# Kernel optimization log

Measured on AMD Instinct MI355X. Metric: run time of the kernel, lower is better.

Reference implementation:

```python
import jax, jax.numpy as jnp
import numpy as np

EPS = 1e-6
WEIGHT_THRESHOLD = 0.0


def setup_inputs() -> dict:
    key = jax.random.key(0)
    kA, kB, kW = jax.random.split(key, 3)
    bs, n = 200000, 20
    A = jax.random.normal(kA, (bs, n, 3), dtype=jnp.float32)
    B = jax.random.normal(kB, (bs, n, 3), dtype=jnp.float32)
    weights = jax.random.uniform(kW, (bs, n), dtype=jnp.float32)
    return {"A": A, "B": B, "weights": weights}


def reference(A, B, weights):
    """Batched weighted Procrustes (Kabsch). A,B: [bs,n,3], weights: [bs,n].
    Returns SE3 transforms [bs,4,4], matching rigid_transform_3d + integrate_trans."""
    w = jnp.where(weights < WEIGHT_THRESHOLD, 0.0, weights)
    wsum = jnp.sum(w, axis=1, keepdims=True)[:, :, None] + EPS  # [bs,1,1]
    centroid_A = jnp.sum(A * w[:, :, None], axis=1, keepdims=True) / wsum  # [bs,1,3]
    centroid_B = jnp.sum(B * w[:, :, None], axis=1, keepdims=True) / wsum
    Am = A - centroid_A
    Bm = B - centroid_B
    # H = Am^T diag(w) Bm  -> [bs,3,3]
    H = jnp.einsum('bni,bn,bnj->bij', Am, w, Bm)
    U, S, Vh = jnp.linalg.svd(H)          # H = U S Vh
    V = jnp.swapaxes(Vh, -1, -2)          # torch.svd's "Vt" is actually V
    Ut = jnp.swapaxes(U, -1, -2)
    delta = jnp.linalg.det(V @ Ut)        # [bs]
    corr = jnp.broadcast_to(jnp.eye(3, dtype=A.dtype), V.shape).copy()
    corr = corr.at[:, 2, 2].set(delta)
    R = V @ corr @ Ut                     # [bs,3,3]
    t = jnp.swapaxes(centroid_B, 1, 2) - R @ jnp.swapaxes(centroid_A, 1, 2)  # [bs,3,1]
    top = jnp.concatenate([R, t], axis=-1)  # [bs,3,4]
    bottom = jnp.broadcast_to(jnp.array([0.0, 0.0, 0.0, 1.0], dtype=A.dtype), (A.shape[0], 1, 4))
    return jnp.concatenate([top, bottom], axis=1)  # [bs,4,4]
```

## Files before the change

### kernel.cpp

```cpp
#include <hip/hip_runtime.h>

#define EPS_W 1e-6f

__global__ __launch_bounds__(256) void kabsch4x4_kernel(
    const float* __restrict__ A, const float* __restrict__ B,
    const float* __restrict__ W, float* __restrict__ Out,
    int bs, int n)
{
    const int b = blockIdx.x * blockDim.x + threadIdx.x;
    if (b >= bs) return;

    float sw = 0.f;
    float Sa0=0.f,Sa1=0.f,Sa2=0.f, Sb0=0.f,Sb1=0.f,Sb2=0.f;
    float M00=0.f,M01=0.f,M02=0.f,M10=0.f,M11=0.f,M12=0.f,M20=0.f,M21=0.f,M22=0.f;

    if ((n & 3) == 0) {
        const float4* A4 = reinterpret_cast<const float4*>(A + (size_t)b * n * 3);
        const float4* B4 = reinterpret_cast<const float4*>(B + (size_t)b * n * 3);
        const float4* W4 = reinterpret_cast<const float4*>(W + (size_t)b * n);
        const int ng = n >> 2;
        for (int g = 0; g < ng; ++g) {
            float4 a0 = A4[3*g+0], a1 = A4[3*g+1], a2 = A4[3*g+2];
            float4 b0 = B4[3*g+0], b1 = B4[3*g+1], b2 = B4[3*g+2];
            float4 wv = W4[g];
            const float af[12] = {a0.x,a0.y,a0.z,a0.w, a1.x,a1.y,a1.z,a1.w, a2.x,a2.y,a2.z,a2.w};
            const float bf[12] = {b0.x,b0.y,b0.z,b0.w, b1.x,b1.y,b1.z,b1.w, b2.x,b2.y,b2.z,b2.w};
            const float wf[4]  = {wv.x,wv.y,wv.z,wv.w};
            #pragma unroll
            for (int k = 0; k < 4; ++k) {
                float w = wf[k] < 0.f ? 0.f : wf[k];
                float ax = af[3*k+0], ay = af[3*k+1], az = af[3*k+2];
                float bx = bf[3*k+0], by = bf[3*k+1], bz = bf[3*k+2];
                sw += w;
                float wax = w*ax, way = w*ay, waz = w*az;
                Sa0 += wax; Sa1 += way; Sa2 += waz;
                Sb0 += w*bx; Sb1 += w*by; Sb2 += w*bz;
                M00 += wax*bx; M01 += wax*by; M02 += wax*bz;
                M10 += way*bx; M11 += way*by; M12 += way*bz;
                M20 += waz*bx; M21 += waz*by; M22 += waz*bz;
            }
        }
    } else {
        for (int j = 0; j < n; ++j) {
            const float* ap = A + ((size_t)b * n + j) * 3;
            const float* bp = B + ((size_t)b * n + j) * 3;
            float w = W[(size_t)b * n + j];
            w = w < 0.f ? 0.f : w;
            float ax=ap[0], ay=ap[1], az=ap[2];
            float bx=bp[0], by=bp[1], bz=bp[2];
            sw += w;
            float wax = w*ax, way = w*ay, waz = w*az;
            Sa0 += wax; Sa1 += way; Sa2 += waz;
            Sb0 += w*bx; Sb1 += w*by; Sb2 += w*bz;
            M00 += wax*bx; M01 += wax*by; M02 += wax*bz;
            M10 += way*bx; M11 += way*by; M12 += way*bz;
            M20 += waz*bx; M21 += waz*by; M22 += waz*bz;
        }
    }

    const float inv = 1.f / (sw + EPS_W);
    const float cA0 = Sa0*inv, cA1 = Sa1*inv, cA2 = Sa2*inv;
    const float cB0 = Sb0*inv, cB1 = Sb1*inv, cB2 = Sb2*inv;

    float H[3][3];
    H[0][0] = M00 - cA0*Sb0 - Sa0*cB0 + sw*cA0*cB0;
    H[0][1] = M01 - cA0*Sb1 - Sa0*cB1 + sw*cA0*cB1;
    H[0][2] = M02 - cA0*Sb2 - Sa0*cB2 + sw*cA0*cB2;
    H[1][0] = M10 - cA1*Sb0 - Sa1*cB0 + sw*cA1*cB0;
    H[1][1] = M11 - cA1*Sb1 - Sa1*cB1 + sw*cA1*cB1;
    H[1][2] = M12 - cA1*Sb2 - Sa1*cB2 + sw*cA1*cB2;
    H[2][0] = M20 - cA2*Sb0 - Sa2*cB0 + sw*cA2*cB0;
    H[2][1] = M21 - cA2*Sb1 - Sa2*cB1 + sw*cA2*cB1;
    H[2][2] = M22 - cA2*Sb2 - Sa2*cB2 + sw*cA2*cB2;

    const float Sxx=H[0][0], Sxy=H[0][1], Sxz=H[0][2];
    const float Syx=H[1][0], Syy=H[1][1], Syz=H[1][2];
    const float Szx=H[2][0], Szy=H[2][1], Szz=H[2][2];

    float Nm[4][4];
    Nm[0][0] =  Sxx+Syy+Szz; Nm[0][1] = Syz-Szy;      Nm[0][2] = Szx-Sxz;      Nm[0][3] = Sxy-Syx;
    Nm[1][0] =  Nm[0][1];    Nm[1][1] = Sxx-Syy-Szz;  Nm[1][2] = Sxy+Syx;      Nm[1][3] = Szx+Sxz;
    Nm[2][0] =  Nm[0][2];    Nm[2][1] = Nm[1][2];     Nm[2][2] = -Sxx+Syy-Szz; Nm[2][3] = Syz+Szy;
    Nm[3][0] =  Nm[0][3];    Nm[3][1] = Nm[1][3];     Nm[3][2] = Nm[2][3];     Nm[3][3] = -Sxx-Syy+Szz;

    float Vv[4][4] = {{1.f,0.f,0.f,0.f},{0.f,1.f,0.f,0.f},{0.f,0.f,1.f,0.f},{0.f,0.f,0.f,1.f}};

    for (int sweep = 0; sweep < 6; ++sweep) {
        #pragma unroll
        for (int pair = 0; pair < 6; ++pair) {
            constexpr int PP[6] = {0,0,0,1,1,2};
            constexpr int QQ[6] = {1,2,3,2,3,3};
            const int p = PP[pair], q = QQ[pair];
            float apq = Nm[p][q];
            float c, s;
            if (fabsf(apq) > 1e-20f) {
                float tau = (Nm[q][q] - Nm[p][p]) / (2.f * apq);
                float t = copysignf(1.f, tau) / (fabsf(tau) + sqrtf(1.f + tau*tau));
                c = rsqrtf(1.f + t*t);
                s = t * c;
            } else {
                c = 1.f; s = 0.f;
            }
            #pragma unroll
            for (int k = 0; k < 4; ++k) {
                float akp = Nm[k][p], akq = Nm[k][q];
                Nm[k][p] = c*akp - s*akq;
                Nm[k][q] = s*akp + c*akq;
            }
            #pragma unroll
            for (int k = 0; k < 4; ++k) {
                float apk = Nm[p][k], aqk = Nm[q][k];
                Nm[p][k] = c*apk - s*aqk;
                Nm[q][k] = s*apk + c*aqk;
            }
            #pragma unroll
            for (int k = 0; k < 4; ++k) {
                float vkp = Vv[k][p], vkq = Vv[k][q];
                Vv[k][p] = c*vkp - s*vkq;
                Vv[k][q] = s*vkp + c*vkq;
            }
        }
    }

    float q0=Vv[0][0], q1=Vv[1][0], q2=Vv[2][0], q3=Vv[3][0];
    float best = Nm[0][0];
    #pragma unroll
    for (int m = 1; m < 4; ++m) {
        bool bt = Nm[m][m] > best;
        best = bt ? Nm[m][m] : best;
        q0 = bt ? Vv[0][m] : q0;
        q1 = bt ? Vv[1][m] : q1;
        q2 = bt ? Vv[2][m] : q2;
        q3 = bt ? Vv[3][m] : q3;
    }
    float qn = rsqrtf(q0*q0 + q1*q1 + q2*q2 + q3*q3);
    q0*=qn; q1*=qn; q2*=qn; q3*=qn;

    float R00 = q0*q0+q1*q1-q2*q2-q3*q3;
    float R01 = 2.f*(q1*q2 - q0*q3);
    float R02 = 2.f*(q1*q3 + q0*q2);
    float R10 = 2.f*(q1*q2 + q0*q3);
    float R11 = q0*q0-q1*q1+q2*q2-q3*q3;
    float R12 = 2.f*(q2*q3 - q0*q1);
    float R20 = 2.f*(q1*q3 - q0*q2);
    float R21 = 2.f*(q2*q3 + q0*q1);
    float R22 = q0*q0-q1*q1-q2*q2+q3*q3;

    float trRH  = R00*H[0][0]+R01*H[1][0]+R02*H[2][0]
                + R10*H[0][1]+R11*H[1][1]+R12*H[2][1]
                + R20*H[0][2]+R21*H[1][2]+R22*H[2][2];
    float trRtH = R00*H[0][0]+R01*H[0][1]+R02*H[0][2]
                + R10*H[1][0]+R11*H[1][1]+R12*H[1][2]
                + R20*H[2][0]+R21*H[2][1]+R22*H[2][2];
    if (trRtH > trRH) {
        float t;
        t = R01; R01 = R10; R10 = t;
        t = R02; R02 = R20; R20 = t;
        t = R12; R12 = R21; R21 = t;
    }

    float t0 = cB0 - (R00*cA0 + R01*cA1 + R02*cA2);
    float t1 = cB1 - (R10*cA0 + R11*cA1 + R12*cA2);
    float t2 = cB2 - (R20*cA0 + R21*cA1 + R22*cA2);

    float4* O4 = reinterpret_cast<float4*>(Out + (size_t)b * 16);
    O4[0] = make_float4(R00, R01, R02, t0);
    O4[1] = make_float4(R10, R11, R12, t1);
    O4[2] = make_float4(R20, R21, R22, t2);
    O4[3] = make_float4(0.f, 0.f, 0.f, 1.f);
}

extern "C" void kernel_launch(void* const* d_in, const int* in_sizes, int n_in,
                              void* d_out, int out_size, void* d_ws, size_t ws_size,
                              hipStream_t stream) {
    const float* A = (const float*)d_in[0];
    const float* B = (const float*)d_in[1];
    const float* W = (const float*)d_in[2];
    float* Out = (float*)d_out;
    const int bs = out_size / 16;
    const int n  = (bs > 0) ? (in_sizes[2] / bs) : 0;
    const int threads = 256;
    const int blocks = (bs + threads - 1) / threads;
    hipLaunchKernelGGL(kabsch4x4_kernel, dim3(blocks), dim3(threads), 0, stream,
                       A, B, W, Out, bs, n);
}
```

Measured before the change: 172.5 us.

## Split each Kabsch item across two lanes, cut Jacobi sweeps, divide-free rotation

For n==20, each batch item is now handled by two adjacent threads. Each thread accumulates half the points with float2 loads, the partial sums are combined with an xor shuffle, and each thread writes half of the 4x4 output. The Jacobi eigen-solve drops from six sweeps to five, and the rotation angle is computed with rsqrt instead of divides and sqrt. The aim is more parallelism and memory-level concurrency for the load phase and less ALU work in the solve. The cost is that both lanes redundantly run the full solve, and the reduced sweep count risks accuracy on ill-conditioned inputs.

```diff
diff --git a/kernel.cpp b/kernel.cpp
--- a/kernel.cpp
+++ b/kernel.cpp
@@ -2,62 +2,14 @@
 
 #define EPS_W 1e-6f
 
-__global__ __launch_bounds__(256) void kabsch4x4_kernel(
-    const float* __restrict__ A, const float* __restrict__ B,
-    const float* __restrict__ W, float* __restrict__ Out,
-    int bs, int n)
+__device__ __forceinline__ void solve_from_sums(
+    float sw, float Sa0, float Sa1, float Sa2,
+    float Sb0, float Sb1, float Sb2,
+    float M00, float M01, float M02,
+    float M10, float M11, float M12,
+    float M20, float M21, float M22,
+    float R[9], float t[3])
 {
-    const int b = blockIdx.x * blockDim.x + threadIdx.x;
-    if (b >= bs) return;
-
-    float sw = 0.f;
-    float Sa0=0.f,Sa1=0.f,Sa2=0.f, Sb0=0.f,Sb1=0.f,Sb2=0.f;
-    float M00=0.f,M01=0.f,M02=0.f,M10=0.f,M11=0.f,M12=0.f,M20=0.f,M21=0.f,M22=0.f;
-
-    if ((n & 3) == 0) {
-        const float4* A4 = reinterpret_cast<const float4*>(A + (size_t)b * n * 3);
-        const float4* B4 = reinterpret_cast<const float4*>(B + (size_t)b * n * 3);
-        const float4* W4 = reinterpret_cast<const float4*>(W + (size_t)b * n);
-        const int ng = n >> 2;
-        for (int g = 0; g < ng; ++g) {
-            float4 a0 = A4[3*g+0], a1 = A4[3*g+1], a2 = A4[3*g+2];
-            float4 b0 = B4[3*g+0], b1 = B4[3*g+1], b2 = B4[3*g+2];
-            float4 wv = W4[g];
-            const float af[12] = {a0.x,a0.y,a0.z,a0.w, a1.x,a1.y,a1.z,a1.w, a2.x,a2.y,a2.z,a2.w};
-            const float bf[12] = {b0.x,b0.y,b0.z,b0.w, b1.x,b1.y,b1.z,b1.w, b2.x,b2.y,b2.z,b2.w};
-            const float wf[4]  = {wv.x,wv.y,wv.z,wv.w};
-            #pragma unroll
-            for (int k = 0; k < 4; ++k) {
-                float w = wf[k] < 0.f ? 0.f : wf[k];
-                float ax = af[3*k+0], ay = af[3*k+1], az = af[3*k+2];
-                float bx = bf[3*k+0], by = bf[3*k+1], bz = bf[3*k+2];
-                sw += w;
-                float wax = w*ax, way = w*ay, waz = w*az;
-                Sa0 += wax; Sa1 += way; Sa2 += waz;
-                Sb0 += w*bx; Sb1 += w*by; Sb2 += w*bz;
-                M00 += wax*bx; M01 += wax*by; M02 += wax*bz;
-                M10 += way*bx; M11 += way*by; M12 += way*bz;
-                M20 += waz*bx; M21 += waz*by; M22 += waz*bz;
-            }
-        }
-    } else {
-        for (int j = 0; j < n; ++j) {
-            const float* ap = A + ((size_t)b * n + j) * 3;
-            const float* bp = B + ((size_t)b * n + j) * 3;
-            float w = W[(size_t)b * n + j];
-            w = w < 0.f ? 0.f : w;
-            float ax=ap[0], ay=ap[1], az=ap[2];
-            float bx=bp[0], by=bp[1], bz=bp[2];
-            sw += w;
-            float wax = w*ax, way = w*ay, waz = w*az;
-            Sa0 += wax; Sa1 += way; Sa2 += waz;
-            Sb0 += w*bx; Sb1 += w*by; Sb2 += w*bz;
-            M00 += wax*bx; M01 += wax*by; M02 += wax*bz;
-            M10 += way*bx; M11 += way*by; M12 += way*bz;
-            M20 += waz*bx; M21 += waz*by; M22 += waz*bz;
-        }
-    }
-
     const float inv = 1.f / (sw + EPS_W);
     const float cA0 = Sa0*inv, cA1 = Sa1*inv, cA2 = Sa2*inv;
     const float cB0 = Sb0*inv, cB1 = Sb1*inv, cB2 = Sb2*inv;
@@ -85,22 +37,23 @@
 
     float Vv[4][4] = {{1.f,0.f,0.f,0.f},{0.f,1.f,0.f,0.f},{0.f,0.f,1.f,0.f},{0.f,0.f,0.f,1.f}};
 
-    for (int sweep = 0; sweep < 6; ++sweep) {
+    for (int sweep = 0; sweep < 5; ++sweep) {
         #pragma unroll
         for (int pair = 0; pair < 6; ++pair) {
             constexpr int PP[6] = {0,0,0,1,1,2};
             constexpr int QQ[6] = {1,2,3,2,3,3};
             const int p = PP[pair], q = QQ[pair];
-            float apq = Nm[p][q];
-            float c, s;
-            if (fabsf(apq) > 1e-20f) {
-                float tau = (Nm[q][q] - Nm[p][p]) / (2.f * apq);
-                float t = copysignf(1.f, tau) / (fabsf(tau) + sqrtf(1.f + tau*tau));
-                c = rsqrtf(1.f + t*t);
-                s = t * c;
-            } else {
-                c = 1.f; s = 0.f;
-            }
+            float d  = Nm[p][p] - Nm[q][q];
+            float o  = Nm[p][q];
+            float r2 = d*d + 4.f*o*o;
+            bool tiny = r2 < 1e-30f;
+            float rinv = rsqrtf(tiny ? 1.f : r2);
+            float hh = 0.5f + 0.5f * fabsf(d) * rinv;
+            float ci = rsqrtf(hh);
+            float c  = hh * ci;
+            float s  = (d < 0.f ? o : -o) * rinv * ci;
+            c = tiny ? 1.f : c;
+            s = tiny ? 0.f : s;
             #pragma unroll
             for (int k = 0; k < 4; ++k) {
                 float akp = Nm[k][p], akq = Nm[k][q];
@@ -153,20 +106,125 @@
                 + R10*H[1][0]+R11*H[1][1]+R12*H[1][2]
                 + R20*H[2][0]+R21*H[2][1]+R22*H[2][2];
     if (trRtH > trRH) {
-        float t;
-        t = R01; R01 = R10; R10 = t;
-        t = R02; R02 = R20; R20 = t;
-        t = R12; R12 = R21; R21 = t;
-    }
-
-    float t0 = cB0 - (R00*cA0 + R01*cA1 + R02*cA2);
-    float t1 = cB1 - (R10*cA0 + R11*cA1 + R12*cA2);
-    float t2 = cB2 - (R20*cA0 + R21*cA1 + R22*cA2);
+        float tt;
+        tt = R01; R01 = R10; R10 = tt;
+        tt = R02; R02 = R20; R20 = tt;
+        tt = R12; R12 = R21; R21 = tt;
+    }
+
+    R[0]=R00; R[1]=R01; R[2]=R02;
+    R[3]=R10; R[4]=R11; R[5]=R12;
+    R[6]=R20; R[7]=R21; R[8]=R22;
+    t[0] = cB0 - (R00*cA0 + R01*cA1 + R02*cA2);
+    t[1] = cB1 - (R10*cA0 + R11*cA1 + R12*cA2);
+    t[2] = cB2 - (R20*cA0 + R21*cA1 + R22*cA2);
+}
+
+__global__ __launch_bounds__(256) void kabsch_pair20_kernel(
+    const float* __restrict__ A, const float* __restrict__ B,
+    const float* __restrict__ W, float* __restrict__ Out, int bs)
+{
+    const int tid  = blockIdx.x * blockDim.x + threadIdx.x;
+    const int item = tid >> 1;
+    const int h    = tid & 1;
+    if (item >= bs) return;
+
+    const float2* A2 = reinterpret_cast<const float2*>(A);
+    const float2* B2 = reinterpret_cast<const float2*>(B);
+    const float2* W2 = reinterpret_cast<const float2*>(W);
+    const int abase = item*30 + h*15;
+    const int wbase = item*10 + h*5;
+
+    float sw = 0.f;
+    float Sa0=0.f,Sa1=0.f,Sa2=0.f, Sb0=0.f,Sb1=0.f,Sb2=0.f;
+    float M00=0.f,M01=0.f,M02=0.f,M10=0.f,M11=0.f,M12=0.f,M20=0.f,M21=0.f,M22=0.f;
+
+    #pragma unroll
+    for (int g = 0; g < 5; ++g) {
+        float2 a0 = A2[abase+3*g+0], a1 = A2[abase+3*g+1], a2 = A2[abase+3*g+2];
+        float2 b0 = B2[abase+3*g+0], b1 = B2[abase+3*g+1], b2 = B2[abase+3*g+2];
+        float2 wv = W2[wbase+g];
+        float w0 = wv.x < 0.f ? 0.f : wv.x;
+        float w1 = wv.y < 0.f ? 0.f : wv.y;
+
+        {
+            float ax=a0.x, ay=a0.y, az=a1.x;
+            float bx=b0.x, by=b0.y, bz=b1.x;
+            sw += w0;
+            float wax=w0*ax, way=w0*ay, waz=w0*az;
+            Sa0+=wax; Sa1+=way; Sa2+=waz;
+            Sb0+=w0*bx; Sb1+=w0*by; Sb2+=w0*bz;
+            M00+=wax*bx; M01+=wax*by; M02+=wax*bz;
+            M10+=way*bx; M11+=way*by; M12+=way*bz;
+            M20+=waz*bx; M21+=waz*by; M22+=waz*bz;
+        }
+        {
+            float ax=a1.y, ay=a2.x, az=a2.y;
+            float bx=b1.y, by=b2.x, bz=b2.y;
+            sw += w1;
+            float wax=w1*ax, way=w1*ay, waz=w1*az;
+            Sa0+=wax; Sa1+=way; Sa2+=waz;
+            Sb0+=w1*bx; Sb1+=w1*by; Sb2+=w1*bz;
+            M00+=wax*bx; M01+=wax*by; M02+=wax*bz;
+            M10+=way*bx; M11+=way*by; M12+=way*bz;
+            M20+=waz*bx; M21+=waz*by; M22+=waz*bz;
+        }
+    }
+
+    sw  += __shfl_xor(sw, 1);
+    Sa0 += __shfl_xor(Sa0,1); Sa1 += __shfl_xor(Sa1,1); Sa2 += __shfl_xor(Sa2,1);
+    Sb0 += __shfl_xor(Sb0,1); Sb1 += __shfl_xor(Sb1,1); Sb2 += __shfl_xor(Sb2,1);
+    M00 += __shfl_xor(M00,1); M01 += __shfl_xor(M01,1); M02 += __shfl_xor(M02,1);
+    M10 += __shfl_xor(M10,1); M11 += __shfl_xor(M11,1); M12 += __shfl_xor(M12,1);
+    M20 += __shfl_xor(M20,1); M21 += __shfl_xor(M21,1); M22 += __shfl_xor(M22,1);
+
+    float R[9], t[3];
+    solve_from_sums(sw,Sa0,Sa1,Sa2,Sb0,Sb1,Sb2,
+                    M00,M01,M02,M10,M11,M12,M20,M21,M22, R, t);
+
+    float4 va = h ? make_float4(R[6],R[7],R[8],t[2]) : make_float4(R[0],R[1],R[2],t[0]);
+    float4 vb = h ? make_float4(0.f,0.f,0.f,1.f)     : make_float4(R[3],R[4],R[5],t[1]);
+    float4* O4 = reinterpret_cast<float4*>(Out + (size_t)item * 16);
+    O4[2*h]   = va;
+    O4[2*h+1] = vb;
+}
+
+__global__ __launch_bounds__(256) void kabsch_generic_kernel(
+    const float* __restrict__ A, const float* __restrict__ B,
+    const float* __restrict__ W, float* __restrict__ Out,
+    int bs, int n)
+{
+    const int b = blockIdx.x * blockDim.x + threadIdx.x;
+    if (b >= bs) return;
+
+    float sw = 0.f;
+    float Sa0=0.f,Sa1=0.f,Sa2=0.f, Sb0=0.f,Sb1=0.f,Sb2=0.f;
+    float M00=0.f,M01=0.f,M02=0.f,M10=0.f,M11=0.f,M12=0.f,M20=0.f,M21=0.f,M22=0.f;
+
+    for (int j = 0; j < n; ++j) {
+        const float* ap = A + ((size_t)b * n + j) * 3;
+        const float* bp = B + ((size_t)b * n + j) * 3;
+        float w = W[(size_t)b * n + j];
+        w = w < 0.f ? 0.f : w;
+        float ax=ap[0], ay=ap[1], az=ap[2];
+        float bx=bp[0], by=bp[1], bz=bp[2];
+        sw += w;
+        float wax = w*ax, way = w*ay, waz = w*az;
+        Sa0 += wax; Sa1 += way; Sa2 += waz;
+        Sb0 += w*bx; Sb1 += w*by; Sb2 += w*bz;
+        M00 += wax*bx; M01 += wax*by; M02 += wax*bz;
+        M10 += way*bx; M11 += way*by; M12 += way*bz;
+        M20 += waz*bx; M21 += waz*by; M22 += waz*bz;
+    }
+
+    float R[9], t[3];
+    solve_from_sums(sw,Sa0,Sa1,Sa2,Sb0,Sb1,Sb2,
+                    M00,M01,M02,M10,M11,M12,M20,M21,M22, R, t);
 
     float4* O4 = reinterpret_cast<float4*>(Out + (size_t)b * 16);
-    O4[0] = make_float4(R00, R01, R02, t0);
-    O4[1] = make_float4(R10, R11, R12, t1);
-    O4[2] = make_float4(R20, R21, R22, t2);
+    O4[0] = make_float4(R[0], R[1], R[2], t[0]);
+    O4[1] = make_float4(R[3], R[4], R[5], t[1]);
+    O4[2] = make_float4(R[6], R[7], R[8], t[2]);
     O4[3] = make_float4(0.f, 0.f, 0.f, 1.f);
 }
 
@@ -180,7 +238,14 @@
     const int bs = out_size / 16;
     const int n  = (bs > 0) ? (in_sizes[2] / bs) : 0;
     const int threads = 256;
-    const int blocks = (bs + threads - 1) / threads;
-    hipLaunchKernelGGL(kabsch4x4_kernel, dim3(blocks), dim3(threads), 0, stream,
-                       A, B, W, Out, bs, n);
-}
+    if (n == 20) {
+        const int total = bs * 2;
+        const int blocks = (total + threads - 1) / threads;
+        hipLaunchKernelGGL(kabsch_pair20_kernel, dim3(blocks), dim3(threads), 0, stream,
+                           A, B, W, Out, bs);
+    } else {
+        const int blocks = (bs + threads - 1) / threads;
+        hipLaunchKernelGGL(kabsch_generic_kernel, dim3(blocks), dim3(threads), 0, stream,
+                           A, B, W, Out, bs, n);
+    }
+}
```

New measurement: 157.1 us. 8.9% less time.
